# Kernel tuning notes

Hardware: AMD Instinct MI355X
Metric: run time of the kernel (lower is better)

## Reference

```python
import jax, jax.numpy as jnp
import numpy as np

EPS = 1e-5
K = 16

gelu = lambda x: jax.nn.gelu(x, approximate=False)

def _ln(x, g, b):
    mu = jnp.mean(x, -1, keepdims=True)
    var = jnp.mean((x - mu) ** 2, -1, keepdims=True)
    return (x - mu) * jax.lax.rsqrt(var + EPS) * g + b

def _bn_last(x, g, b, m, v):  # BN over channels-last axis (eval mode, running stats)
    return (x - m) * jax.lax.rsqrt(v + EPS) * g + b

def _bn_c(x, g, b, m, v):  # x [B,C,T]
    return (x - m[None, :, None]) * jax.lax.rsqrt(v + EPS)[None, :, None] * g[None, :, None] + b[None, :, None]

def _conv1d(x, w, b, pad):  # x [B,C,T], w [O,I,W]
    y = jax.lax.conv_general_dilated(x, w, (1,), [(pad, pad)], dimension_numbers=('NCH', 'OIH', 'NCH'))
    return y + b[None, :, None]

def _edge_conv(x, ew1, eg1, eb1, em1, ev1, ew2, eg2, eb2, em2, ev2):
    # x: [BT,P,C]; kNN in xyz (first 3 channels), gather neighbors, edge MLP, max over k
    xyz = x[..., :3]
    sq = jnp.sum(xyz * xyz, -1)
    d = sq[:, :, None] + sq[:, None, :] - 2.0 * jnp.einsum('bpc,bqc->bpq', xyz, xyz)
    _, idx = jax.lax.top_k(-d, K)                       # k smallest distances (incl. self)
    x_j = jax.vmap(lambda xb, ib: xb[ib])(x, idx)       # [BT,P,K,C]
    x_i = jnp.broadcast_to(x[:, :, None, :], x_j.shape)
    edge = jnp.concatenate([x_i, x_j - x_i], -1)        # [BT,P,K,2C]
    h = gelu(_bn_last(jnp.einsum('bpke,oe->bpko', edge, ew1), eg1, eb1, em1, ev1))
    h = gelu(_bn_last(jnp.einsum('bpko,qo->bpkq', h, ew2), eg2, eb2, em2, ev2))
    return jnp.max(h, axis=2)                           # [BT,P,128]

def setup_inputs():
    key = jax.random.key(0)
    ks = iter(jax.random.split(key, 80))
    def r(shape, s=0.05):
        return jax.random.normal(next(ks), shape, jnp.float32) * s
    d = {}
    d['x_pt'] = jax.random.normal(next(ks), (8, 32, 256, 10), jnp.float32)
    d['x_fr'] = jax.random.normal(next(ks), (8, 32, 4), jnp.float32)
    d['ew1'] = r((64, 20), 0.1)
    d['eg1'], d['eb1'], d['em1'], d['ev1'] = jnp.ones(64), jnp.zeros(64), r((64,)), jnp.ones(64)
    d['ew2'] = r((128, 64), 0.1)
    d['eg2'], d['eb2'], d['em2'], d['ev2'] = jnp.ones(128), jnp.zeros(128), r((128,)), jnp.ones(128)
    d['p1w'], d['p1b'] = r((138, 128), 0.08), r((128,))
    d['ln1g'], d['ln1b'] = jnp.ones(128), jnp.zeros(128)
    d['p2w'], d['p2b'] = r((128, 256), 0.08), r((256,))
    d['ln2g'], d['ln2b'] = jnp.ones(256), jnp.zeros(256)
    d['f1w'], d['f1b'] = r((4, 32), 0.3), r((32,))
    d['f2w'], d['f2b'] = r((32, 64), 0.15), r((64,))
    d['projw'], d['projb'] = r((256, 576, 1), 0.04), r((256,))
    for i in (1, 2, 3, 4):
        d['c%dw' % i], d['c%db' % i] = r((256, 256, 3), 0.03), r((256,))
        d['g%d' % i], d['be%d' % i], d['m%d' % i], d['v%d' % i] = jnp.ones(256), jnp.zeros(256), r((256,)), jnp.ones(256)
    d['h1w'], d['h1b'] = r((256, 128), 0.08), r((128,))
    d['h2w'], d['h2b'] = r((128, 25), 0.08), r((25,))
    return d

def reference(x_pt, x_fr, ew1, eg1, eb1, em1, ev1, ew2, eg2, eb2, em2, ev2, p1w, p1b, ln1g, ln1b, p2w, p2b, ln2g, ln2b, f1w, f1b, f2w, f2b, projw, projb, c1w, c1b, g1, be1, m1, v1, c2w, c2b, g2, be2, m2, v2, c3w, c3b, g3, be3, m3, v3, c4w, c4b, g4, be4, m4, v4, h1w, h1b, h2w, h2b):
    B, T, P, C = x_pt.shape
    x_bt = x_pt.reshape(B * T, P, C)
    local = _edge_conv(x_bt, ew1, eg1, eb1, em1, ev1, ew2, eg2, eb2, em2, ev2)
    h = jnp.concatenate([local, x_bt], -1)              # [BT,P,138]
    h = gelu(_ln(h @ p1w + p1b, ln1g, ln1b))
    h = gelu(_ln(h @ p2w + p2b, ln2g, ln2b))
    h = h.reshape(B, T, P, 256)
    pf = jnp.concatenate([jnp.max(h, 2), jnp.mean(h, 2)], -1)  # [B,T,512]
    fr = gelu(x_fr @ f1w + f1b) @ f2w + f2b                    # [B,T,64]
    per = jnp.concatenate([pf, fr], -1)                        # [B,T,576]
    hs = jnp.transpose(per, (0, 2, 1))                         # [B,576,T]
    hs = _conv1d(hs, projw, projb, 0)
    hs = gelu(_bn_c(_conv1d(hs, c1w, c1b, 1), g1, be1, m1, v1))
    hs = hs + gelu(_bn_c(_conv1d(hs, c2w, c2b, 1), g2, be2, m2, v2))
    hs = hs + gelu(_bn_c(_conv1d(hs, c3w, c3b, 1), g3, be3, m3, v3))
    hs = hs + gelu(_bn_c(_conv1d(hs, c4w, c4b, 1), g4, be4, m4, v4))
    pooled = jnp.max(hs, -1)                                   # [B,256]
    return gelu(pooled @ h1w + h1b) @ h2w + h2b                # [B,25]
```

## Files before the change

kernel.cpp:

```cpp
#include <hip/hip_runtime.h>
#include <math.h>

#define NBT   256
#define NP    256
#define NC    10
#define KNN   16
#define NPB   8

typedef unsigned short ushort_t;
typedef unsigned char uchar_t;
typedef __attribute__((ext_vector_type(8))) short short8;
typedef __attribute__((ext_vector_type(4))) float f32x4;

__device__ __forceinline__ float gelu_f(float x) {
  return 0.5f * x * (1.0f + erff(x * 0.7071067811865476f));
}
__device__ __forceinline__ float gelu_fast(float x) {
  float u  = x * 0.7071067811865476f;
  float au = fabsf(u);
  float t  = __builtin_amdgcn_rcpf(fmaf(0.3275911f, au, 1.0f));
  float p  = fmaf(t, 1.061405429f, -1.453152027f);
  p = fmaf(t, p, 1.421413741f);
  p = fmaf(t, p, -0.284496736f);
  p = fmaf(t, p, 0.254829592f);
  p = p * t;
  float e  = __expf(-au * au);
  float er = fmaf(-p, e, 1.0f);
  er = copysignf(er, u);
  return 0.5f * x * (1.0f + er);
}
__device__ __forceinline__ ushort_t f2bf(float f) {
  unsigned u = __float_as_uint(f);
  return (ushort_t)((u + 0x7FFFu + ((u >> 16) & 1u)) >> 16);
}

__global__ __launch_bounds__(256) void knn_kernel(const float* __restrict__ x_pt,
                                                  uchar_t* __restrict__ idx) {
  __shared__ float sx[NP], sy[NP], sz[NP], ssq[NP];
  int bt = blockIdx.x >> 6;
  int p0 = (blockIdx.x & 63) * 4;
  int tid = threadIdx.x;
  const float* xb = x_pt + (size_t)bt * NP * NC;
  {
    int q = tid;
    float x0 = xb[q*NC+0], x1 = xb[q*NC+1], x2 = xb[q*NC+2];
    sx[q] = x0; sy[q] = x1; sz[q] = x2;
    ssq[q] = x0*x0 + x1*x1 + x2*x2;
  }
  __syncthreads();

  int wv = tid >> 6, lane = tid & 63;
  int p = p0 + wv;
  float px = sx[p], py = sy[p], pz = sz[p], psq = ssq[p];

  unsigned k0, k1, k2, k3;
  {
    unsigned kk[4];
#pragma unroll
    for (int c = 0; c < 4; ++c) {
      int q = lane + c*64;
      float d = psq + ssq[q] - 2.0f*(px*sx[q] + py*sy[q] + pz*sz[q]);
      d = fmaxf(d, 0.0f);
      kk[c] = (__float_as_uint(d) & 0xFFFFFF00u) | (unsigned)q;
    }
    unsigned a0 = min(kk[0], kk[1]), a1 = max(kk[0], kk[1]);
    unsigned a2 = min(kk[2], kk[3]), a3 = max(kk[2], kk[3]);
    unsigned b0 = min(a0, a2), b2 = max(a0, a2);
    unsigned b1 = min(a1, a3), b3 = max(a1, a3);
    k0 = b0; k1 = min(b1, b2); k2 = max(b1, b2); k3 = b3;
  }

  unsigned cur = k0, mykeep = 0u;
#pragma unroll
  for (int r = 0; r < 16; ++r) {
    unsigned w = cur;
    w = min(w, (unsigned)__shfl_xor((int)w, 1));
    w = min(w, (unsigned)__shfl_xor((int)w, 2));
    w = min(w, (unsigned)__shfl_xor((int)w, 4));
    w = min(w, (unsigned)__shfl_xor((int)w, 8));
    w = min(w, (unsigned)__shfl_xor((int)w, 16));
    w = min(w, (unsigned)__shfl_xor((int)w, 32));
    bool win = (cur == w);
    cur = win ? k1 : cur;
    k1  = win ? k2 : k1;
    k2  = win ? k3 : k2;
    k3  = win ? 0xFFFFFFFFu : k3;
    if (lane == r) mykeep = w;
  }
  if (lane < 16)
    idx[((size_t)bt*NP + p)*KNN + lane] = (uchar_t)(mykeep & 0xFFu);
}

__global__ __launch_bounds__(256) void featAB_kernel(const float* __restrict__ x_pt,
                                                     const float* __restrict__ ew1,
                                                     float* __restrict__ Af,
                                                     float* __restrict__ Bf) {
  int t = blockIdx.x*256 + threadIdx.x;
  int o = t & 63, p = t >> 6;
  const float* xr = x_pt + (size_t)p*NC;
  float a = 0.f, b = 0.f;
#pragma unroll
  for (int e = 0; e < NC; ++e) {
    float w1 = ew1[o*20 + e], w2 = ew1[o*20 + 10 + e];
    float xv = xr[e];
    a = fmaf(xv, w1 - w2, a);
    b = fmaf(xv, w2, b);
  }
  Af[(size_t)p*64 + o] = a;
  Bf[(size_t)p*64 + o] = b;
}

__global__ __launch_bounds__(256) void prep_kernel(
    const float* __restrict__ p1w, const float* __restrict__ p2w,
    const float* __restrict__ ew2,
    ushort_t* __restrict__ w1b, ushort_t* __restrict__ w2b,
    ushort_t* __restrict__ ew2b) {
  int i = blockIdx.x*256 + threadIdx.x;
  if (i < 21504) {
    int o = i / 168, e = i - o*168;
    w1b[i] = f2bf((e < 138) ? p1w[e*128 + o] : 0.f);
  } else if (i < 56320) {
    int j = i - 21504;
    int q = j / 136, e = j - q*136;
    w2b[j] = f2bf((e < 128) ? p2w[e*256 + q] : 0.f);
  } else {
    int m = i - 56320;
    int q = m / 72, o = m - q*72;
    ew2b[m] = f2bf((o < 64) ? ew2[q*64 + o] : 0.f);
  }
}

__global__ __launch_bounds__(256, 2) void edgeconv_kernel(
    const float* __restrict__ Af, const float* __restrict__ Bf,
    const uchar_t* __restrict__ idx, const ushort_t* __restrict__ ew2b,
    const float* __restrict__ eg1, const float* __restrict__ eb1,
    const float* __restrict__ em1, const float* __restrict__ ev1,
    const float* __restrict__ eg2, const float* __restrict__ eb2,
    const float* __restrict__ em2, const float* __restrict__ ev2,
    float* __restrict__ localf) {
  __shared__ __align__(16) ushort_t h1s[128*72];
  __shared__ __align__(16) ushort_t w2T[128*72];
  __shared__ float sc1[64], sh1[64], sc2[128], sh2[128];
  __shared__ int idxs[128];

  int tid = threadIdx.x;
  int bid = blockIdx.x;
  int wid = (bid & 7) * 1024 + (bid >> 3);
  int p0  = wid * NPB;
  int bt  = p0 >> 8;

  for (int i = tid; i < 1152; i += 256)
    ((uint4*)w2T)[i] = ((const uint4*)ew2b)[i];
  if (tid < 128) idxs[tid] = idx[(size_t)p0*16 + tid];
  if (tid < 64) {
    float s = eg1[tid] * (1.0f / sqrtf(ev1[tid] + 1e-5f));
    sc1[tid] = s; sh1[tid] = eb1[tid] - em1[tid]*s;
  }
  if (tid >= 64 && tid < 192) {
    int q = tid - 64;
    float s = eg2[q] * (1.0f / sqrtf(ev2[q] + 1e-5f));
    sc2[q] = s; sh2[q] = eb2[q] - em2[q]*s;
  }
  __syncthreads();

  {
    int o = tid & 63, g = tid >> 6;
    float s1 = sc1[o], h1v = sh1[o];
    const float* Bbase = Bf + (size_t)bt*NP*64 + o;
#pragma unroll
    for (int pi = 0; pi < 2; ++pi) {
      int pt = g*2 + pi;
      float af = Af[((size_t)(p0+pt))*64 + o];
      ushort_t* hrow = h1s + (pt*16)*72 + o;
      for (int k = 0; k < KNN; ++k) {
        int j = idxs[pt*16 + k];
        float hv = af + Bbase[(size_t)j*64];
        hrow[k*72] = f2bf(gelu_fast(fmaf(hv, s1, h1v)));
      }
    }
  }
  __syncthreads();

  int w = tid >> 6, l = tid & 63;
  int m_lo = l & 15, kq = l >> 4;

  short8 afr[2][2];
#pragma unroll
  for (int pt = 0; pt < 2; ++pt)
#pragma unroll
    for (int ks = 0; ks < 2; ++ks)
      afr[pt][ks] = *(const short8*)&h1s[((2*w+pt)*16 + m_lo)*72 + ks*32 + kq*8];

  f32x4 acc[2][8];
#pragma unroll
  for (int pt = 0; pt < 2; ++pt)
#pragma unroll
    for (int ct = 0; ct < 8; ++ct) acc[pt][ct] = (f32x4){0.f,0.f,0.f,0.f};

#pragma unroll
  for (int ct = 0; ct < 8; ++ct) {
#pragma unroll
    for (int ks = 0; ks < 2; ++ks) {
      short8 bfr = *(const short8*)&w2T[(ct*16 + m_lo)*72 + ks*32 + kq*8];
      acc[0][ct] = __builtin_amdgcn_mfma_f32_16x16x32_bf16(afr[0][ks], bfr, acc[0][ct], 0, 0, 0);
      acc[1][ct] = __builtin_amdgcn_mfma_f32_16x16x32_bf16(afr[1][ks], bfr, acc[1][ct], 0, 0, 0);
    }
  }

#pragma unroll
  for (int pt = 0; pt < 2; ++pt) {
    int gp = p0 + 2*w + pt;
#pragma unroll
    for (int ct = 0; ct < 8; ++ct) {
      int q = ct*16 + m_lo;
      float sc = sc2[q], sh = sh2[q];
      f32x4 a = acc[pt][ct];
      float mn = INFINITY, mx = -INFINITY;
#pragma unroll
      for (int r = 0; r < 4; ++r) {
        float y = fmaf(a[r], sc, sh);
        mn = fminf(mn, y); mx = fmaxf(mx, y);
      }
      mn = fminf(mn, __shfl_xor(mn, 16));
      mn = fminf(mn, __shfl_xor(mn, 32));
      mx = fmaxf(mx, __shfl_xor(mx, 16));
      mx = fmaxf(mx, __shfl_xor(mx, 32));
      float g = gelu_fast((kq & 1) ? mx : mn);
      g = fmaxf(g, __shfl_xor(g, 16));
      if (l < 16)
        localf[(size_t)gp*128 + q] = g;
    }
  }
}

__global__ __launch_bounds__(256, 2) void p1p2_kernel(
    const float* __restrict__ localf, const float* __restrict__ x_pt,
    const ushort_t* __restrict__ w1b, const ushort_t* __restrict__ w2b,
    const float* __restrict__ p1b,
    const float* __restrict__ ln1g, const float* __restrict__ ln1b,
    const float* __restrict__ p2b,
    const float* __restrict__ ln2g, const float* __restrict__ ln2b,
    float* __restrict__ pmaxb, float* __restrict__ psumb) {
  __shared__ __align__(16) ushort_t sA[64*168];
  __shared__ __align__(16) ushort_t wt[128*168];
  __shared__ float pm4[4*256], ps4[4*256];
  int blk = blockIdx.x;
  int bt = blk >> 2, ch = blk & 3;
  int tid = threadIdx.x;
  size_t gbase = (size_t)bt*NP + ch*64;

  for (int i = tid; i < 64*32; i += 256) {
    int pp = i >> 5, v = i & 31;
    float4 f4 = *(const float4*)(localf + (gbase+pp)*128 + v*4);
    ushort_t* dst = sA + pp*168 + v*4;
    dst[0]=f2bf(f4.x); dst[1]=f2bf(f4.y); dst[2]=f2bf(f4.z); dst[3]=f2bf(f4.w);
  }
  for (int i = tid; i < 64*40; i += 256) {
    int pp = i / 40, e = i - pp*40;
    ushort_t v = 0;
    if (e < 10) v = f2bf(x_pt[(gbase+pp)*NC + e]);
    sA[pp*168 + 128 + e] = v;
  }
  for (int i = tid; i < 2688; i += 256)
    ((uint4*)wt)[i] = ((const uint4*)w1b)[i];
  __syncthreads();

  int w = tid >> 6, l = tid & 63;
  int lo = l & 15, kq = l >> 4;

  short8 af1[5];
#pragma unroll
  for (int ks = 0; ks < 5; ++ks)
    af1[ks] = *(const short8*)&sA[(w*16 + lo)*168 + ks*32 + kq*8];
  f32x4 acc1[8];
#pragma unroll
  for (int ct = 0; ct < 8; ++ct) {
    float b = p1b[ct*16 + lo];
    acc1[ct] = (f32x4){b, b, b, b};
  }
#pragma unroll
  for (int ct = 0; ct < 8; ++ct) {
#pragma unroll
    for (int ks = 0; ks < 5; ++ks) {
      short8 bf = *(const short8*)&wt[(ct*16 + lo)*168 + ks*32 + kq*8];
      acc1[ct] = __builtin_amdgcn_mfma_f32_16x16x32_bf16(af1[ks], bf, acc1[ct], 0, 0, 0);
    }
  }
  __syncthreads();

  {
    float g1v[8], b1v[8];
#pragma unroll
    for (int ct = 0; ct < 8; ++ct) { g1v[ct] = ln1g[ct*16+lo]; b1v[ct] = ln1b[ct*16+lo]; }
#pragma unroll
    for (int r = 0; r < 4; ++r) {
      float s = 0.f;
#pragma unroll
      for (int ct = 0; ct < 8; ++ct) s += acc1[ct][r];
      s += __shfl_xor(s,1); s += __shfl_xor(s,2); s += __shfl_xor(s,4); s += __shfl_xor(s,8);
      float mu = s * (1.0f/128.0f);
      float s2 = 0.f;
#pragma unroll
      for (int ct = 0; ct < 8; ++ct) { float d = acc1[ct][r]-mu; s2 += d*d; }
      s2 += __shfl_xor(s2,1); s2 += __shfl_xor(s2,2); s2 += __shfl_xor(s2,4); s2 += __shfl_xor(s2,8);
      float rs = 1.0f / sqrtf(s2*(1.0f/128.0f) + 1e-5f);
      int row = w*16 + kq*4 + r;
#pragma unroll
      for (int ct = 0; ct < 8; ++ct) {
        float h = gelu_fast((acc1[ct][r]-mu)*rs*g1v[ct] + b1v[ct]);
        sA[row*168 + ct*16 + lo] = f2bf(h);
      }
    }
  }
  for (int i = tid; i < 2176; i += 256)
    ((uint4*)wt)[i] = ((const uint4*)w2b)[i];
  __syncthreads();

  short8 af2[4];
#pragma unroll
  for (int ks = 0; ks < 4; ++ks)
    af2[ks] = *(const short8*)&sA[(w*16 + lo)*168 + ks*32 + kq*8];
  f32x4 acc2[16];
#pragma unroll
  for (int ct = 0; ct < 8; ++ct) {
    float bA = p2b[ct*16 + lo], bB = p2b[128 + ct*16 + lo];
    acc2[ct]   = (f32x4){bA, bA, bA, bA};
    acc2[8+ct] = (f32x4){bB, bB, bB, bB};
  }
#pragma unroll
  for (int ct = 0; ct < 8; ++ct) {
#pragma unroll
    for (int ks = 0; ks < 4; ++ks) {
      short8 bf = *(const short8*)&wt[(ct*16 + lo)*136 + ks*32 + kq*8];
      acc2[ct] = __builtin_amdgcn_mfma_f32_16x16x32_bf16(af2[ks], bf, acc2[ct], 0, 0, 0);
    }
  }
  __syncthreads();
  for (int i = tid; i < 2176; i += 256)
    ((uint4*)wt)[i] = ((const uint4*)(w2b + 17408))[i];
  __syncthreads();
#pragma unroll
  for (int ct = 0; ct < 8; ++ct) {
#pragma unroll
    for (int ks = 0; ks < 4; ++ks) {
      short8 bf = *(const short8*)&wt[(ct*16 + lo)*136 + ks*32 + kq*8];
      acc2[8+ct] = __builtin_amdgcn_mfma_f32_16x16x32_bf16(af2[ks], bf, acc2[8+ct], 0, 0, 0);
    }
  }

  float vmax[16], vsum[16];
  {
    float g2v[16], b2v[16];
#pragma unroll
    for (int j = 0; j < 16; ++j) {
      int c = (j >= 8 ? 128 : 0) + (j & 7)*16 + lo;
      g2v[j] = ln2g[c]; b2v[j] = ln2b[c];
    }
#pragma unroll
    for (int j = 0; j < 16; ++j) { vmax[j] = -INFINITY; vsum[j] = 0.f; }
#pragma unroll
    for (int r = 0; r < 4; ++r) {
      float s = 0.f;
#pragma unroll
      for (int j = 0; j < 16; ++j) s += acc2[j][r];
      s += __shfl_xor(s,1); s += __shfl_xor(s,2); s += __shfl_xor(s,4); s += __shfl_xor(s,8);
      float mu = s * (1.0f/256.0f);
      float s2 = 0.f;
#pragma unroll
      for (int j = 0; j < 16; ++j) { float d = acc2[j][r]-mu; s2 += d*d; }
      s2 += __shfl_xor(s2,1); s2 += __shfl_xor(s2,2); s2 += __shfl_xor(s2,4); s2 += __shfl_xor(s2,8);
      float rs = 1.0f / sqrtf(s2*(1.0f/256.0f) + 1e-5f);
#pragma unroll
      for (int j = 0; j < 16; ++j) {
        float v = gelu_fast((acc2[j][r]-mu)*rs*g2v[j] + b2v[j]);
        vmax[j] = fmaxf(vmax[j], v);
        vsum[j] += v;
      }
    }
  }
#pragma unroll
  for (int j = 0; j < 16; ++j) {
    float m = vmax[j], s = vsum[j];
    m = fmaxf(m, __shfl_xor(m, 16)); m = fmaxf(m, __shfl_xor(m, 32));
    s += __shfl_xor(s, 16);          s += __shfl_xor(s, 32);
    if (l < 16) {
      int c = (j >= 8 ? 128 : 0) + (j & 7)*16 + l;
      pm4[w*256 + c] = m;
      ps4[w*256 + c] = s;
    }
  }
  __syncthreads();
  {
    int c = tid;
    float mx = fmaxf(fmaxf(pm4[c], pm4[256+c]), fmaxf(pm4[512+c], pm4[768+c]));
    float sm = ps4[c] + ps4[256+c] + ps4[512+c] + ps4[768+c];
    pmaxb[(size_t)blk*256 + c] = mx;
    psumb[(size_t)blk*256 + c] = sm;
  }
}

__global__ __launch_bounds__(256) void p1p2_reduce_kernel(
    const float* __restrict__ pmaxb, const float* __restrict__ psumb,
    const float* __restrict__ xfr, const float* __restrict__ f1w,
    const float* __restrict__ f1b, const float* __restrict__ f2w,
    const float* __restrict__ f2b, float* __restrict__ perbuf) {
  int bt = blockIdx.x, q = threadIdx.x;
  const float* mb = pmaxb + (size_t)bt*4*256 + q;
  const float* sb = psumb + (size_t)bt*4*256 + q;
  float mx = -INFINITY, sm = 0.f;
#pragma unroll
  for (int i = 0; i < 4; ++i) {
    mx = fmaxf(mx, mb[i*256]);
    sm += sb[i*256];
  }
  perbuf[(size_t)bt*576 + q] = mx;
  perbuf[(size_t)bt*576 + 256 + q] = sm * (1.0f/256.0f);

  if (q < 64) {
    float x0 = xfr[bt*4], x1 = xfr[bt*4+1], x2 = xfr[bt*4+2], x3 = xfr[bt*4+3];
    float acc = f2b[q];
#pragma unroll
    for (int e = 0; e < 32; ++e) {
      float hv = f1b[e];
      hv = fmaf(x0, f1w[e], hv);
      hv = fmaf(x1, f1w[32+e], hv);
      hv = fmaf(x2, f1w[64+e], hv);
      hv = fmaf(x3, f1w[96+e], hv);
      acc = fmaf(gelu_f(hv), f2w[e*64 + q], acc);
    }
    perbuf[(size_t)bt*576 + 512 + q] = acc;
  }
}

__global__ __launch_bounds__(256) void proj_kernel(
    const float* __restrict__ per, const float* __restrict__ projw,
    const float* __restrict__ projb, float* __restrict__ hout) {
  __shared__ __align__(16) float sp[576];
  int bt = blockIdx.x, c = threadIdx.x;
  for (int i = c; i < 576; i += 256) sp[i] = per[(size_t)bt*576 + i];
  __syncthreads();
  float acc = projb[c];
  const float* wr = projw + (size_t)c*576;
  for (int i = 0; i < 144; ++i) {
    float4 wv = *(const float4*)(wr + i*4);
    float4 pv = *(const float4*)(sp + i*4);
    acc = fmaf(wv.x, pv.x, acc); acc = fmaf(wv.y, pv.y, acc);
    acc = fmaf(wv.z, pv.z, acc); acc = fmaf(wv.w, pv.w, acc);
  }
  hout[(size_t)bt*256 + c] = acc;
}

__global__ __launch_bounds__(256) void conv_bn_kernel(
    const float* __restrict__ hin, float* __restrict__ hout,
    const float* __restrict__ w, const float* __restrict__ bias,
    const float* __restrict__ g, const float* __restrict__ be,
    const float* __restrict__ m, const float* __restrict__ v,
    int residual) {
  __shared__ __align__(16) float win[768];
  int bt = blockIdx.x, b = bt >> 5, t = bt & 31;
  int c = threadIdx.x;
  for (int i = c; i < 768; i += 256) {
    int cin = i / 3, dt = i - cin*3;
    int tt = t + dt - 1;
    win[i] = (tt >= 0 && tt < 32) ? hin[((size_t)b*32 + tt)*256 + cin] : 0.0f;
  }
  __syncthreads();
  float acc = bias[c];
  const float* wr = w + (size_t)c*768;
  for (int i = 0; i < 192; ++i) {
    float4 wv = *(const float4*)(wr + i*4);
    float4 pv = *(const float4*)(win + i*4);
    acc = fmaf(wv.x, pv.x, acc); acc = fmaf(wv.y, pv.y, acc);
    acc = fmaf(wv.z, pv.z, acc); acc = fmaf(wv.w, pv.w, acc);
  }
  float rsv = 1.0f / sqrtf(v[c] + 1e-5f);
  float y = (acc - m[c]) * rsv * g[c] + be[c];
  y = gelu_f(y);
  if (residual) y += win[c*3 + 1];
  hout[(size_t)bt*256 + c] = y;
}

__global__ __launch_bounds__(256) void poolhead_kernel(
    const float* __restrict__ hs, const float* __restrict__ h1w,
    const float* __restrict__ h1b, const float* __restrict__ h2w,
    const float* __restrict__ h2b, float* __restrict__ out) {
  __shared__ float pooled[256];
  __shared__ float hh[128];
  int b = blockIdx.x, tid = threadIdx.x;
  float mx = -INFINITY;
  for (int t = 0; t < 32; ++t)
    mx = fmaxf(mx, hs[((size_t)b*32 + t)*256 + tid]);
  pooled[tid] = mx;
  __syncthreads();
  if (tid < 128) {
    float acc = h1b[tid];
    for (int e = 0; e < 256; ++e) acc = fmaf(pooled[e], h1w[e*128 + tid], acc);
    hh[tid] = gelu_f(acc);
  }
  __syncthreads();
  if (tid < 25) {
    float acc = h2b[tid];
    for (int e = 0; e < 128; ++e) acc = fmaf(hh[e], h2w[e*25 + tid], acc);
    out[b*25 + tid] = acc;
  }
}

extern "C" void kernel_launch(void* const* d_in, const int* in_sizes, int n_in,
                              void* d_out, int out_size, void* d_ws, size_t ws_size,
                              hipStream_t stream) {
  const float* x_pt = (const float*)d_in[0];
  const float* x_fr = (const float*)d_in[1];
  const float* ew1  = (const float*)d_in[2];
  const float* eg1  = (const float*)d_in[3];
  const float* eb1  = (const float*)d_in[4];
  const float* em1  = (const float*)d_in[5];
  const float* ev1  = (const float*)d_in[6];
  const float* ew2  = (const float*)d_in[7];
  const float* eg2  = (const float*)d_in[8];
  const float* eb2  = (const float*)d_in[9];
  const float* em2  = (const float*)d_in[10];
  const float* ev2  = (const float*)d_in[11];
  const float* p1w  = (const float*)d_in[12];
  const float* p1b  = (const float*)d_in[13];
  const float* ln1g = (const float*)d_in[14];
  const float* ln1b = (const float*)d_in[15];
  const float* p2w  = (const float*)d_in[16];
  const float* p2b  = (const float*)d_in[17];
  const float* ln2g = (const float*)d_in[18];
  const float* ln2b = (const float*)d_in[19];
  const float* f1w  = (const float*)d_in[20];
  const float* f1b  = (const float*)d_in[21];
  const float* f2w  = (const float*)d_in[22];
  const float* f2b  = (const float*)d_in[23];
  const float* projw= (const float*)d_in[24];
  const float* projb= (const float*)d_in[25];
  const float* cw[4] = {(const float*)d_in[26],(const float*)d_in[32],(const float*)d_in[38],(const float*)d_in[44]};
  const float* cb[4] = {(const float*)d_in[27],(const float*)d_in[33],(const float*)d_in[39],(const float*)d_in[45]};
  const float* cg[4] = {(const float*)d_in[28],(const float*)d_in[34],(const float*)d_in[40],(const float*)d_in[46]};
  const float* cbe[4]= {(const float*)d_in[29],(const float*)d_in[35],(const float*)d_in[41],(const float*)d_in[47]};
  const float* cm[4] = {(const float*)d_in[30],(const float*)d_in[36],(const float*)d_in[42],(const float*)d_in[48]};
  const float* cv[4] = {(const float*)d_in[31],(const float*)d_in[37],(const float*)d_in[43],(const float*)d_in[49]};
  const float* h1w  = (const float*)d_in[50];
  const float* h1b  = (const float*)d_in[51];
  const float* h2w  = (const float*)d_in[52];
  const float* h2b  = (const float*)d_in[53];
  float* out = (float*)d_out;

  char* ws = (char*)d_ws;
  uchar_t* idxw  = (uchar_t*)ws;
  float* perbuf  = (float*)ws;
  float* hs0     = (float*)(ws + 0x90000);
  float* hs1     = (float*)(ws + 0x90000 + 0x40000);
  float* hs2     = (float*)(ws + 0x90000 + 2*0x40000);
  float* hs3     = (float*)(ws + 0x90000 + 3*0x40000);
  float* hs4     = (float*)(ws + 0x90000 + 4*0x40000);
  ushort_t* ew2b = (ushort_t*)(ws + 0x200000);
  ushort_t* w1b  = (ushort_t*)(ws + 0x200000 + 0x8000);
  ushort_t* w2b  = (ushort_t*)(ws + 0x200000 + 0x14000);
  float* Af      = (float*)(ws + ((size_t)4  << 20));
  float* Bfw     = (float*)(ws + ((size_t)20 << 20));
  float* localf  = (float*)(ws + ((size_t)36 << 20));
  float* pmaxb   = (float*)(ws + ((size_t)8  << 20));
  float* psumb   = (float*)(ws + ((size_t)12 << 20));

  knn_kernel<<<NBT*64, 256, 0, stream>>>(x_pt, idxw);
  featAB_kernel<<<(NBT*NP*64)/256, 256, 0, stream>>>(x_pt, ew1, Af, Bfw);
  prep_kernel<<<256, 256, 0, stream>>>(p1w, p2w, ew2, w1b, w2b, ew2b);
  edgeconv_kernel<<<(NBT*NP)/NPB, 256, 0, stream>>>(Af, Bfw, idxw, ew2b,
      eg1, eb1, em1, ev1, eg2, eb2, em2, ev2, localf);
  p1p2_kernel<<<NBT*4, 256, 0, stream>>>(localf, x_pt, w1b, w2b, p1b,
      ln1g, ln1b, p2b, ln2g, ln2b, pmaxb, psumb);
  p1p2_reduce_kernel<<<NBT, 256, 0, stream>>>(pmaxb, psumb, x_fr,
      f1w, f1b, f2w, f2b, perbuf);
  proj_kernel<<<NBT, 256, 0, stream>>>(perbuf, projw, projb, hs0);
  conv_bn_kernel<<<NBT, 256, 0, stream>>>(hs0, hs1, cw[0], cb[0], cg[0], cbe[0], cm[0], cv[0], 0);
  conv_bn_kernel<<<NBT, 256, 0, stream>>>(hs1, hs2, cw[1], cb[1], cg[1], cbe[1], cm[1], cv[1], 1);
  conv_bn_kernel<<<NBT, 256, 0, stream>>>(hs2, hs3, cw[2], cb[2], cg[2], cbe[2], cm[2], cv[2], 1);
  conv_bn_kernel<<<NBT, 256, 0, stream>>>(hs3, hs4, cw[3], cb[3], cg[3], cbe[3], cm[3], cv[3], 1);
  poolhead_kernel<<<8, 256, 0, stream>>>(hs4, h1w, h1b, h2w, h2b, out);
}
```

Before: 523.4 us.

## Fuse projection, conv/BN stack and head into one MFMA tail kernel; bf16 local features

```diff
diff --git a/kernel.cpp b/kernel.cpp
--- a/kernel.cpp
+++ b/kernel.cpp
@@ -130,6 +130,47 @@
   }
 }
 
+__global__ __launch_bounds__(256) void prep2_kernel(
+    const float* __restrict__ projw,
+    const float* __restrict__ cw0, const float* __restrict__ cw1,
+    const float* __restrict__ cw2, const float* __restrict__ cw3,
+    const float* __restrict__ cb0, const float* __restrict__ cb1,
+    const float* __restrict__ cb2, const float* __restrict__ cb3,
+    const float* __restrict__ cg0, const float* __restrict__ cg1,
+    const float* __restrict__ cg2, const float* __restrict__ cg3,
+    const float* __restrict__ be0, const float* __restrict__ be1,
+    const float* __restrict__ be2, const float* __restrict__ be3,
+    const float* __restrict__ cm0, const float* __restrict__ cm1,
+    const float* __restrict__ cm2, const float* __restrict__ cm3,
+    const float* __restrict__ cv0, const float* __restrict__ cv1,
+    const float* __restrict__ cv2, const float* __restrict__ cv3,
+    ushort_t* __restrict__ pjb, ushort_t* __restrict__ cwb,
+    float* __restrict__ SCt, float* __restrict__ SHt) {
+  const float* cwp[4] = {cw0, cw1, cw2, cw3};
+  const float* cbp[4] = {cb0, cb1, cb2, cb3};
+  const float* cgp[4] = {cg0, cg1, cg2, cg3};
+  const float* bep[4] = {be0, be1, be2, be3};
+  const float* cmp[4] = {cm0, cm1, cm2, cm3};
+  const float* cvp[4] = {cv0, cv1, cv2, cv3};
+  int i = blockIdx.x*256 + threadIdx.x;
+  if (i < 147456) {
+    pjb[i] = f2bf(projw[i]);
+  } else if (i < 147456 + 786432) {
+    int j = i - 147456;
+    int lay = j / 196608, rem = j - lay*196608;
+    int c = rem / 768, kp = rem - c*768;
+    int dt = kp >> 8, cin = kp & 255;
+    cwb[j] = f2bf(cwp[lay][c*768 + cin*3 + dt]);
+  } else if (i < 147456 + 786432 + 1024) {
+    int j = i - 147456 - 786432;
+    int lay = j >> 8, c = j & 255;
+    float rsv = 1.0f / sqrtf(cvp[lay][c] + 1e-5f);
+    float sc = cgp[lay][c] * rsv;
+    SCt[j] = sc;
+    SHt[j] = (cbp[lay][c] - cmp[lay][c]) * sc + bep[lay][c];
+  }
+}
+
 __global__ __launch_bounds__(256, 2) void edgeconv_kernel(
     const float* __restrict__ Af, const float* __restrict__ Bf,
     const uchar_t* __restrict__ idx, const ushort_t* __restrict__ ew2b,
@@ -137,7 +178,7 @@
     const float* __restrict__ em1, const float* __restrict__ ev1,
     const float* __restrict__ eg2, const float* __restrict__ eb2,
     const float* __restrict__ em2, const float* __restrict__ ev2,
-    float* __restrict__ localf) {
+    ushort_t* __restrict__ localfb) {
   __shared__ __align__(16) ushort_t h1s[128*72];
   __shared__ __align__(16) ushort_t w2T[128*72];
   __shared__ float sc1[64], sh1[64], sc2[128], sh2[128];
@@ -172,6 +213,7 @@
       int pt = g*2 + pi;
       float af = Af[((size_t)(p0+pt))*64 + o];
       ushort_t* hrow = h1s + (pt*16)*72 + o;
+#pragma unroll
       for (int k = 0; k < KNN; ++k) {
         int j = idxs[pt*16 + k];
         float hv = af + Bbase[(size_t)j*64];
@@ -228,13 +270,13 @@
       float g = gelu_fast((kq & 1) ? mx : mn);
       g = fmaxf(g, __shfl_xor(g, 16));
       if (l < 16)
-        localf[(size_t)gp*128 + q] = g;
+        localfb[(size_t)gp*128 + q] = f2bf(g);
     }
   }
 }
 
 __global__ __launch_bounds__(256, 2) void p1p2_kernel(
-    const float* __restrict__ localf, const float* __restrict__ x_pt,
+    const ushort_t* __restrict__ localfb, const float* __restrict__ x_pt,
     const ushort_t* __restrict__ w1b, const ushort_t* __restrict__ w2b,
     const float* __restrict__ p1b,
     const float* __restrict__ ln1g, const float* __restrict__ ln1b,
@@ -249,11 +291,10 @@
   int tid = threadIdx.x;
   size_t gbase = (size_t)bt*NP + ch*64;
 
-  for (int i = tid; i < 64*32; i += 256) {
-    int pp = i >> 5, v = i & 31;
-    float4 f4 = *(const float4*)(localf + (gbase+pp)*128 + v*4);
-    ushort_t* dst = sA + pp*168 + v*4;
-    dst[0]=f2bf(f4.x); dst[1]=f2bf(f4.y); dst[2]=f2bf(f4.z); dst[3]=f2bf(f4.w);
+  for (int i = tid; i < 1024; i += 256) {
+    int pp = i >> 4, v = i & 15;
+    *(uint4*)(sA + pp*168 + v*8) =
+        *(const uint4*)(localfb + (gbase+pp)*128 + v*8);
   }
   for (int i = tid; i < 64*40; i += 256) {
     int pp = i / 40, e = i - pp*40;
@@ -432,65 +473,101 @@
   }
 }
 
-__global__ __launch_bounds__(256) void proj_kernel(
-    const float* __restrict__ per, const float* __restrict__ projw,
-    const float* __restrict__ projb, float* __restrict__ hout) {
-  __shared__ __align__(16) float sp[576];
-  int bt = blockIdx.x, c = threadIdx.x;
-  for (int i = c; i < 576; i += 256) sp[i] = per[(size_t)bt*576 + i];
-  __syncthreads();
-  float acc = projb[c];
-  const float* wr = projw + (size_t)c*576;
-  for (int i = 0; i < 144; ++i) {
-    float4 wv = *(const float4*)(wr + i*4);
-    float4 pv = *(const float4*)(sp + i*4);
-    acc = fmaf(wv.x, pv.x, acc); acc = fmaf(wv.y, pv.y, acc);
-    acc = fmaf(wv.z, pv.z, acc); acc = fmaf(wv.w, pv.w, acc);
-  }
-  hout[(size_t)bt*256 + c] = acc;
-}
-
-__global__ __launch_bounds__(256) void conv_bn_kernel(
-    const float* __restrict__ hin, float* __restrict__ hout,
-    const float* __restrict__ w, const float* __restrict__ bias,
-    const float* __restrict__ g, const float* __restrict__ be,
-    const float* __restrict__ m, const float* __restrict__ v,
-    int residual) {
-  __shared__ __align__(16) float win[768];
-  int bt = blockIdx.x, b = bt >> 5, t = bt & 31;
-  int c = threadIdx.x;
-  for (int i = c; i < 768; i += 256) {
-    int cin = i / 3, dt = i - cin*3;
-    int tt = t + dt - 1;
-    win[i] = (tt >= 0 && tt < 32) ? hin[((size_t)b*32 + tt)*256 + cin] : 0.0f;
-  }
-  __syncthreads();
-  float acc = bias[c];
-  const float* wr = w + (size_t)c*768;
-  for (int i = 0; i < 192; ++i) {
-    float4 wv = *(const float4*)(wr + i*4);
-    float4 pv = *(const float4*)(win + i*4);
-    acc = fmaf(wv.x, pv.x, acc); acc = fmaf(wv.y, pv.y, acc);
-    acc = fmaf(wv.z, pv.z, acc); acc = fmaf(wv.w, pv.w, acc);
-  }
-  float rsv = 1.0f / sqrtf(v[c] + 1e-5f);
-  float y = (acc - m[c]) * rsv * g[c] + be[c];
-  y = gelu_f(y);
-  if (residual) y += win[c*3 + 1];
-  hout[(size_t)bt*256 + c] = y;
-}
-
-__global__ __launch_bounds__(256) void poolhead_kernel(
-    const float* __restrict__ hs, const float* __restrict__ h1w,
-    const float* __restrict__ h1b, const float* __restrict__ h2w,
-    const float* __restrict__ h2b, float* __restrict__ out) {
-  __shared__ float pooled[256];
-  __shared__ float hh[128];
+__global__ __launch_bounds__(512, 1) void tail_kernel(
+    const float* __restrict__ perbuf,
+    const ushort_t* __restrict__ pjb, const ushort_t* __restrict__ cwb,
+    const float* __restrict__ projb,
+    const float* __restrict__ SCt, const float* __restrict__ SHt,
+    const float* __restrict__ h1w, const float* __restrict__ h1b,
+    const float* __restrict__ h2w, const float* __restrict__ h2b,
+    float* __restrict__ out) {
+  __shared__ __align__(16) ushort_t perA[32*584];
+  __shared__ __align__(16) float master[32*260];
+  __shared__ __align__(16) ushort_t hsb[34*264];
+  __shared__ float pooled[256], hh[128];
   int b = blockIdx.x, tid = threadIdx.x;
-  float mx = -INFINITY;
-  for (int t = 0; t < 32; ++t)
-    mx = fmaxf(mx, hs[((size_t)b*32 + t)*256 + tid]);
-  pooled[tid] = mx;
+  int w = tid >> 6, l = tid & 63;
+  int lo = l & 15, kq = l >> 4;
+  int mt = w & 1, nq = w >> 1;
+
+  for (int i = tid; i < 4608; i += 512) {
+    int t = i / 144, v = i - t*144;
+    float4 f4 = *(const float4*)(perbuf + ((size_t)b*32 + t)*576 + v*4);
+    ushort_t* dst = perA + t*584 + v*4;
+    dst[0]=f2bf(f4.x); dst[1]=f2bf(f4.y); dst[2]=f2bf(f4.z); dst[3]=f2bf(f4.w);
+  }
+  for (int i = tid; i < 264; i += 512) { hsb[i] = 0; hsb[33*264 + i] = 0; }
+  __syncthreads();
+
+  {
+    f32x4 acc[4];
+#pragma unroll
+    for (int j = 0; j < 4; ++j) {
+      float bb = projb[(nq*4+j)*16 + lo];
+      acc[j] = (f32x4){bb, bb, bb, bb};
+    }
+    for (int ks = 0; ks < 18; ++ks) {
+      short8 af = *(const short8*)&perA[(mt*16 + lo)*584 + ks*32 + kq*8];
+#pragma unroll
+      for (int j = 0; j < 4; ++j) {
+        int ct = nq*4 + j;
+        short8 bf = *(const short8*)&pjb[(ct*16 + lo)*576 + ks*32 + kq*8];
+        acc[j] = __builtin_amdgcn_mfma_f32_16x16x32_bf16(af, bf, acc[j], 0, 0, 0);
+      }
+    }
+#pragma unroll
+    for (int j = 0; j < 4; ++j) {
+      int col = (nq*4+j)*16 + lo;
+#pragma unroll
+      for (int r = 0; r < 4; ++r)
+        master[(mt*16 + kq*4 + r)*260 + col] = acc[j][r];
+    }
+  }
+  __syncthreads();
+
+  for (int lay = 0; lay < 4; ++lay) {
+    for (int i = tid; i < 8192; i += 512) {
+      int t = i >> 8, c = i & 255;
+      hsb[(t+1)*264 + c] = f2bf(master[t*260 + c]);
+    }
+    __syncthreads();
+
+    f32x4 acc[4];
+#pragma unroll
+    for (int j = 0; j < 4; ++j) acc[j] = (f32x4){0.f,0.f,0.f,0.f};
+    const ushort_t* wb = cwb + (size_t)lay*196608;
+    for (int ks = 0; ks < 24; ++ks) {
+      int dt = ks >> 3, cin0 = (ks & 7)*32 + kq*8;
+      short8 af = *(const short8*)&hsb[(mt*16 + lo + dt)*264 + cin0];
+#pragma unroll
+      for (int j = 0; j < 4; ++j) {
+        int ct = nq*4 + j;
+        short8 bf = *(const short8*)&wb[(ct*16 + lo)*768 + ks*32 + kq*8];
+        acc[j] = __builtin_amdgcn_mfma_f32_16x16x32_bf16(af, bf, acc[j], 0, 0, 0);
+      }
+    }
+    __syncthreads();
+#pragma unroll
+    for (int j = 0; j < 4; ++j) {
+      int col = (nq*4+j)*16 + lo;
+      float sc = SCt[lay*256 + col], sh = SHt[lay*256 + col];
+#pragma unroll
+      for (int r = 0; r < 4; ++r) {
+        int row = mt*16 + kq*4 + r;
+        float y = gelu_fast(fmaf(acc[j][r], sc, sh));
+        if (lay > 0) y += master[row*260 + col];
+        master[row*260 + col] = y;
+      }
+    }
+    __syncthreads();
+  }
+
+  if (tid < 256) {
+    float mx = -INFINITY;
+#pragma unroll 8
+    for (int t = 0; t < 32; ++t) mx = fmaxf(mx, master[t*260 + tid]);
+    pooled[tid] = mx;
+  }
   __syncthreads();
   if (tid < 128) {
     float acc = h1b[tid];
@@ -549,33 +626,33 @@
   char* ws = (char*)d_ws;
   uchar_t* idxw  = (uchar_t*)ws;
   float* perbuf  = (float*)ws;
-  float* hs0     = (float*)(ws + 0x90000);
-  float* hs1     = (float*)(ws + 0x90000 + 0x40000);
-  float* hs2     = (float*)(ws + 0x90000 + 2*0x40000);
-  float* hs3     = (float*)(ws + 0x90000 + 3*0x40000);
-  float* hs4     = (float*)(ws + 0x90000 + 4*0x40000);
   ushort_t* ew2b = (ushort_t*)(ws + 0x200000);
   ushort_t* w1b  = (ushort_t*)(ws + 0x200000 + 0x8000);
   ushort_t* w2b  = (ushort_t*)(ws + 0x200000 + 0x14000);
-  float* Af      = (float*)(ws + ((size_t)4  << 20));
-  float* Bfw     = (float*)(ws + ((size_t)20 << 20));
-  float* localf  = (float*)(ws + ((size_t)36 << 20));
-  float* pmaxb   = (float*)(ws + ((size_t)8  << 20));
-  float* psumb   = (float*)(ws + ((size_t)12 << 20));
+  ushort_t* pjb  = (ushort_t*)(ws + 0x200000 + 0x28000);
+  ushort_t* cwb  = (ushort_t*)(ws + 0x200000 + 0x70000);
+  float* SCt     = (float*)(ws + 0x200000 + 0x1F0000);
+  float* SHt     = (float*)(ws + 0x200000 + 0x1F1000);
+  float* pmaxb   = (float*)(ws + ((size_t)4  << 20));
+  float* psumb   = (float*)(ws + ((size_t)6  << 20));
+  float* Af      = (float*)(ws + ((size_t)12 << 20));
+  float* Bfw     = (float*)(ws + ((size_t)28 << 20));
+  ushort_t* localfb = (ushort_t*)(ws + ((size_t)44 << 20));
 
   knn_kernel<<<NBT*64, 256, 0, stream>>>(x_pt, idxw);
   featAB_kernel<<<(NBT*NP*64)/256, 256, 0, stream>>>(x_pt, ew1, Af, Bfw);
   prep_kernel<<<256, 256, 0, stream>>>(p1w, p2w, ew2, w1b, w2b, ew2b);
+  prep2_kernel<<<3656, 256, 0, stream>>>(projw,
+      cw[0], cw[1], cw[2], cw[3], cb[0], cb[1], cb[2], cb[3],
+      cg[0], cg[1], cg[2], cg[3], cbe[0], cbe[1], cbe[2], cbe[3],
+      cm[0], cm[1], cm[2], cm[3], cv[0], cv[1], cv[2], cv[3],
+      pjb, cwb, SCt, SHt);
   edgeconv_kernel<<<(NBT*NP)/NPB, 256, 0, stream>>>(Af, Bfw, idxw, ew2b,
-      eg1, eb1, em1, ev1, eg2, eb2, em2, ev2, localf);
-  p1p2_kernel<<<NBT*4, 256, 0, stream>>>(localf, x_pt, w1b, w2b, p1b,
+      eg1, eb1, em1, ev1, eg2, eb2, em2, ev2, localfb);
+  p1p2_kernel<<<NBT*4, 256, 0, stream>>>(localfb, x_pt, w1b, w2b, p1b,
       ln1g, ln1b, p2b, ln2g, ln2b, pmaxb, psumb);
   p1p2_reduce_kernel<<<NBT, 256, 0, stream>>>(pmaxb, psumb, x_fr,
       f1w, f1b, f2w, f2b, perbuf);
-  proj_kernel<<<NBT, 256, 0, stream>>>(perbuf, projw, projb, hs0);
-  conv_bn_kernel<<<NBT, 256, 0, stream>>>(hs0, hs1, cw[0], cb[0], cg[0], cbe[0], cm[0], cv[0], 0);
-  conv_bn_kernel<<<NBT, 256, 0, stream>>>(hs1, hs2, cw[1], cb[1], cg[1], cbe[1], cm[1], cv[1], 1);
-  conv_bn_kernel<<<NBT, 256, 0, stream>>>(hs2, hs3, cw[2], cb[2], cg[2], cbe[2], cm[2], cv[2], 1);
-  conv_bn_kernel<<<NBT, 256, 0, stream>>>(hs3, hs4, cw[3], cb[3], cg[3], cbe[3], cm[3], cv[3], 1);
-  poolhead_kernel<<<8, 256, 0, stream>>>(hs4, h1w, h1b, h2w, h2b, out);
-}
+  tail_kernel<<<8, 512, 0, stream>>>(perbuf, pjb, cwb, projb, SCt, SHt,
+      h1w, h1b, h2w, h2b, out);
+}
```

New measurement: 518.3 us. No clear change (-1.0%).
